# Performance work log

Measured on AMD Instinct MI355X. Metric: run time of the kernel, lower is better.

The kernel has to match this reference:

```python
import jax, jax.numpy as jnp
import numpy as np

L = 4          # decomposition_levels
PRUNE_Q = 0.4  # pruning_ratio


def haar_dwt2(img):
    a = img[:, 0::2, 0::2]; b = img[:, 0::2, 1::2]
    c = img[:, 1::2, 0::2]; d = img[:, 1::2, 1::2]
    cA = (a + b + c + d) * 0.5
    cH = (a - b + c - d) * 0.5
    cV = (a + b - c - d) * 0.5
    cD = (a - b - c + d) * 0.5
    return cA, cH, cV, cD


def haar_idwt2(cA, cH, cV, cD):
    # exact inverse of haar_dwt2: [B, h, w] -> [B, 2h, 2w]
    a = (cA + cH + cV + cD) * 0.5
    b = (cA - cH + cV - cD) * 0.5
    c = (cA + cH - cV - cD) * 0.5
    d = (cA - cH - cV + cD) * 0.5
    B, h, w = cA.shape
    top = jnp.stack([a, b], axis=-1).reshape(B, h, 2 * w)  # interleave cols
    bot = jnp.stack([c, d], axis=-1).reshape(B, h, 2 * w)
    return jnp.stack([top, bot], axis=2).reshape(B, 2 * h, 2 * w)  # interleave rows


def setup_inputs() -> dict:
    key = jax.random.key(0)
    k1, k2, k3 = jax.random.split(key, 3)
    B, in_dim, out_dim = 128, 4096, 4096
    x = jax.random.normal(k1, (B, in_dim), jnp.float32)
    base_weight = jax.random.normal(k2, (out_dim, in_dim), jnp.float32) * 0.02
    bias = jax.random.normal(k3, (out_dim,), jnp.float32) * 0.02
    scale_factors = jnp.ones((L, 4), jnp.float32)  # per-level, per-subband
    return {"x": x, "base_weight": base_weight, "bias": bias,
            "scale_factors": scale_factors}


def reference(x, base_weight, bias, scale_factors):
    B, in_dim = x.shape
    S = int(np.sqrt(in_dim))  # 64: each sample viewed as SxS image
    base_out = x @ base_weight.T  # [B, out_dim]

    # multi-level Haar analysis with per-level scaling + quantile pruning
    cA = x.reshape(B, S, S)
    levels = []
    for l in range(L):
        cA, cH, cV, cD = haar_dwt2(cA)
        co = jnp.stack([cA, cH, cV, cD], axis=1)  # [B, 4, h, w]
        co = co * scale_factors[l][None, :, None, None]
        ab = jnp.abs(co)
        thr = jnp.quantile(ab, PRUNE_Q, axis=-1, keepdims=True)
        co = co * (ab > thr).astype(co.dtype)
        levels.append(co)

    # synthesis from pruned coefficients
    rec = levels[-1][:, 0]  # coarsest pruned cA
    for l in range(L - 1, -1, -1):
        rec = haar_idwt2(rec, levels[l][:, 1], levels[l][:, 2], levels[l][:, 3])

    wavelet_out = rec.reshape(B, in_dim)  # out_dim == in_dim
    return base_out + wavelet_out + bias
```

## Files before the change

kernel.cpp:

```cpp
#include <hip/hip_runtime.h>
#include <hip/hip_bf16.h>

typedef __attribute__((ext_vector_type(8))) short bf16x8;
typedef __attribute__((ext_vector_type(4))) float f32x4;

__device__ __forceinline__ unsigned short f2bf(float f) {
  unsigned int u = __float_as_uint(f);
  u += 0x7FFFu + ((u >> 16) & 1u);
  return (unsigned short)(u >> 16);
}

__host__ __device__ constexpr int prOffset(int l) {
  return (l == 0) ? 0 : (l == 1) ? 3072 : (l == 2) ? 3840 : 4032;
}

template<int N>
__device__ __forceinline__ float row_thr(const float* __restrict__ row, float sc) {
  float v[N];
#pragma unroll
  for (int j = 0; j < N; ++j) v[j] = fabsf(row[j] * sc);
  constexpr float p = 0.4f * (float)(N - 1);
  constexpr int k = (int)p;
  constexpr float frac = p - (float)k;
  float vlo = 0.f, vhi = 0.f;
  for (int i = 0; i < N; ++i) {
    const float vi = fabsf(row[i] * sc);
    int clt = 0, ceq = 0;
#pragma unroll
    for (int j = 0; j < N; ++j) {
      clt += (v[j] < vi) ? 1 : 0;
      ceq += (v[j] == vi) ? 1 : 0;
    }
    if (clt <= k && k < clt + ceq) vlo = vi;
    if (clt <= k + 1 && (k + 1) < clt + ceq) vhi = vi;
  }
  return vlo * (1.0f - frac) + vhi * frac;
}

__global__ __launch_bounds__(256) void wavelet_kernel(
    const float* __restrict__ x,
    const float* __restrict__ bias,
    const float* __restrict__ scl,
    float* __restrict__ out) {
  __shared__ float cur[4096];
  __shared__ float tmp[4096];
  __shared__ float pr[4096];
  const int b = blockIdx.x;
  const int tid = threadIdx.x;
  const float* xi = x + (size_t)b * 4096;

  for (int i = tid; i < 4096; i += 256) cur[i] = xi[i];
  __syncthreads();

  int h = 64;
#pragma unroll
  for (int l = 0; l < 4; ++l) {
    const int half = h >> 1;
    const int hh = half * half;
    for (int e = tid; e < hh; e += 256) {
      const int i = e / half, j = e - i * half;
      const float a  = cur[(i * 2) * h + j * 2];
      const float bb = cur[(i * 2) * h + j * 2 + 1];
      const float c  = cur[(i * 2 + 1) * h + j * 2];
      const float d  = cur[(i * 2 + 1) * h + j * 2 + 1];
      tmp[e]          = (((a + bb) + c) + d) * 0.5f;
      tmp[hh + e]     = (((a - bb) + c) - d) * 0.5f;
      tmp[2 * hh + e] = (((a + bb) - c) - d) * 0.5f;
      tmp[3 * hh + e] = (((a - bb) - c) + d) * 0.5f;
    }
    __syncthreads();
    const int nrows = 4 * half;
    if (tid < nrows) {
      const int s = tid / half, i = tid - s * half;
      const float sc = scl[l * 4 + s];
      const float* row = &tmp[s * hh + i * half];
      float thr;
      if (half == 32)      thr = row_thr<32>(row, sc);
      else if (half == 16) thr = row_thr<16>(row, sc);
      else if (half == 8)  thr = row_thr<8>(row, sc);
      else                 thr = row_thr<4>(row, sc);
      float* dst = nullptr;
      if (s >= 1)          dst = &pr[prOffset(l) + (s - 1) * hh + i * half];
      else if (l == 3)     dst = &pr[4080 + i * 4];
      if (dst) {
        for (int j = 0; j < half; ++j) {
          const float co = row[j] * sc;
          dst[j] = (fabsf(co) > thr) ? co : 0.0f;
        }
      }
    }
    for (int e = tid; e < hh; e += 256) cur[e] = tmp[e];
    __syncthreads();
    h = half;
  }

#pragma unroll
  for (int l = 3; l >= 0; --l) {
    const int half = 64 >> (l + 1);
    const int hh = half * half;
    const int po = prOffset(l);
    const float* src = (l == 3) ? &pr[4080] : ((l & 1) ? tmp : cur);
    float* dst = (l & 1) ? cur : tmp;
    const int W2 = half * 2;
    for (int e = tid; e < hh; e += 256) {
      const int i = e / half, j = e - i * half;
      const float cA = src[e];
      const float cH = pr[po + 0 * hh + i * half + j];
      const float cV = pr[po + 1 * hh + i * half + j];
      const float cD = pr[po + 2 * hh + i * half + j];
      const float a2 = (((cA + cH) + cV) + cD) * 0.5f;
      const float b2 = (((cA - cH) + cV) - cD) * 0.5f;
      const float c2 = (((cA + cH) - cV) - cD) * 0.5f;
      const float d2 = (((cA - cH) - cV) + cD) * 0.5f;
      dst[(i * 2) * W2 + j * 2]         = a2;
      dst[(i * 2) * W2 + j * 2 + 1]     = b2;
      dst[(i * 2 + 1) * W2 + j * 2]     = c2;
      dst[(i * 2 + 1) * W2 + j * 2 + 1] = d2;
    }
    __syncthreads();
  }
  float* o = out + (size_t)b * 4096;
  for (int e = tid; e < 4096; e += 256) o[e] = tmp[e] + bias[e];
}

__global__ __launch_bounds__(256, 2) void gemm_kernel(
    const float* __restrict__ x,
    const float* __restrict__ w,
    float* __restrict__ out) {
  __shared__ __align__(16) unsigned short Asm[2][128][40];
  __shared__ __align__(16) unsigned short Bsm[2][64][40];
  const int tid = threadIdx.x;
  const int nt = blockIdx.x & 63;
  const int ks = blockIdx.x >> 6;
  const int n0 = nt * 64;
  const int k0 = ks * 512;
  const int q = tid & 7;
  const int r0 = tid >> 3;
  const int lane = tid & 63, wid = tid >> 6;
  const int wm = wid >> 1, wn = wid & 1;
  const int fr = lane & 15;
  const int k8 = (lane >> 4) * 8;

  f32x4 acc[4][2];
#pragma unroll
  for (int mi = 0; mi < 4; ++mi)
#pragma unroll
    for (int ni = 0; ni < 2; ++ni)
      acc[mi][ni] = f32x4{0.f, 0.f, 0.f, 0.f};

  float4 ra[4];
  float4 rb[2];
#pragma unroll
  for (int p = 0; p < 4; ++p)
    ra[p] = *(const float4*)&x[(size_t)(r0 + p * 32) * 4096 + k0 + q * 4];
#pragma unroll
  for (int p = 0; p < 2; ++p)
    rb[p] = *(const float4*)&w[(size_t)(n0 + r0 + p * 32) * 4096 + k0 + q * 4];
#pragma unroll
  for (int p = 0; p < 4; ++p) {
    ushort4 pk = {f2bf(ra[p].x), f2bf(ra[p].y), f2bf(ra[p].z), f2bf(ra[p].w)};
    *(ushort4*)&Asm[0][r0 + p * 32][q * 4] = pk;
  }
#pragma unroll
  for (int p = 0; p < 2; ++p) {
    ushort4 pk = {f2bf(rb[p].x), f2bf(rb[p].y), f2bf(rb[p].z), f2bf(rb[p].w)};
    *(ushort4*)&Bsm[0][r0 + p * 32][q * 4] = pk;
  }
  __syncthreads();

  for (int t = 0; t < 16; ++t) {
    const int cb = t & 1;
    if (t < 15) {
      const int kg = k0 + (t + 1) * 32;
#pragma unroll
      for (int p = 0; p < 4; ++p)
        ra[p] = *(const float4*)&x[(size_t)(r0 + p * 32) * 4096 + kg + q * 4];
#pragma unroll
      for (int p = 0; p < 2; ++p)
        rb[p] = *(const float4*)&w[(size_t)(n0 + r0 + p * 32) * 4096 + kg + q * 4];
    }
    bf16x8 af[4], bg[2];
#pragma unroll
    for (int mi = 0; mi < 4; ++mi)
      af[mi] = *(const bf16x8*)&Asm[cb][wm * 64 + mi * 16 + fr][k8];
#pragma unroll
    for (int ni = 0; ni < 2; ++ni)
      bg[ni] = *(const bf16x8*)&Bsm[cb][wn * 32 + ni * 16 + fr][k8];
#pragma unroll
    for (int mi = 0; mi < 4; ++mi)
#pragma unroll
      for (int ni = 0; ni < 2; ++ni)
        acc[mi][ni] = __builtin_amdgcn_mfma_f32_16x16x32_bf16(
            af[mi], bg[ni], acc[mi][ni], 0, 0, 0);
    if (t < 15) {
#pragma unroll
      for (int p = 0; p < 4; ++p) {
        ushort4 pk = {f2bf(ra[p].x), f2bf(ra[p].y), f2bf(ra[p].z), f2bf(ra[p].w)};
        *(ushort4*)&Asm[cb ^ 1][r0 + p * 32][q * 4] = pk;
      }
#pragma unroll
      for (int p = 0; p < 2; ++p) {
        ushort4 pk = {f2bf(rb[p].x), f2bf(rb[p].y), f2bf(rb[p].z), f2bf(rb[p].w)};
        *(ushort4*)&Bsm[cb ^ 1][r0 + p * 32][q * 4] = pk;
      }
    }
    __syncthreads();
  }

  const int rbase = wm * 64 + (lane >> 4) * 4;
  const int cbase = n0 + wn * 32 + fr;
#pragma unroll
  for (int mi = 0; mi < 4; ++mi)
#pragma unroll
    for (int ni = 0; ni < 2; ++ni)
#pragma unroll
      for (int j = 0; j < 4; ++j)
        atomicAdd(&out[(size_t)(rbase + mi * 16 + j) * 4096 + cbase + ni * 16],
                  acc[mi][ni][j]);
}

extern "C" void kernel_launch(void* const* d_in, const int* in_sizes, int n_in,
                              void* d_out, int out_size, void* d_ws, size_t ws_size,
                              hipStream_t stream) {
  const float* x    = (const float*)d_in[0];
  const float* w    = (const float*)d_in[1];
  const float* bias = (const float*)d_in[2];
  const float* scl  = (const float*)d_in[3];
  float* out = (float*)d_out;
  hipLaunchKernelGGL(wavelet_kernel, dim3(128), dim3(256), 0, stream,
                     x, bias, scl, out);
  hipLaunchKernelGGL(gemm_kernel, dim3(512), dim3(256), 0, stream,
                     x, w, out);
}
```

Before: 155.5 us.

## Parallelize quantile thresholds and add LDS-free GEMM on pre-converted bf16 activations

The per-row quantile threshold, previously one thread per row doing an O(N^2) rank count, is now spread across all 256 threads: each thread ranks a few elements and the row's low and high order statistics are written to shared memory. The wavelet kernel also writes a bf16 copy of x into the workspace, which a new GEMM kernel reads straight from global memory into MFMA fragments. That kernel converts weights with packed cvt instructions and uses no shared memory or barriers. This aims to cut the serial threshold latency and the LDS staging and conversion overhead in the GEMM, in exchange for a GEMM that now depends on the wavelet kernel and needs enough workspace.

```diff
diff --git a/kernel.cpp b/kernel.cpp
--- a/kernel.cpp
+++ b/kernel.cpp
@@ -10,89 +10,115 @@
   return (unsigned short)(u >> 16);
 }
 
+__device__ __forceinline__ bf16x8 pack8(float4 lo, float4 hi) {
+  union { unsigned int u[4]; bf16x8 v; } r;
+  asm("v_cvt_pk_bf16_f32 %0, %1, %2" : "=v"(r.u[0]) : "v"(lo.x), "v"(lo.y));
+  asm("v_cvt_pk_bf16_f32 %0, %1, %2" : "=v"(r.u[1]) : "v"(lo.z), "v"(lo.w));
+  asm("v_cvt_pk_bf16_f32 %0, %1, %2" : "=v"(r.u[2]) : "v"(hi.x), "v"(hi.y));
+  asm("v_cvt_pk_bf16_f32 %0, %1, %2" : "=v"(r.u[3]) : "v"(hi.z), "v"(hi.w));
+  return r.v;
+}
+
 __host__ __device__ constexpr int prOffset(int l) {
   return (l == 0) ? 0 : (l == 1) ? 3072 : (l == 2) ? 3840 : 4032;
 }
 
-template<int N>
-__device__ __forceinline__ float row_thr(const float* __restrict__ row, float sc) {
-  float v[N];
-#pragma unroll
-  for (int j = 0; j < N; ++j) v[j] = fabsf(row[j] * sc);
-  constexpr float p = 0.4f * (float)(N - 1);
-  constexpr int k = (int)p;
-  constexpr float frac = p - (float)k;
-  float vlo = 0.f, vhi = 0.f;
-  for (int i = 0; i < N; ++i) {
-    const float vi = fabsf(row[i] * sc);
-    int clt = 0, ceq = 0;
-#pragma unroll
-    for (int j = 0; j < N; ++j) {
-      clt += (v[j] < vi) ? 1 : 0;
-      ceq += (v[j] == vi) ? 1 : 0;
-    }
-    if (clt <= k && k < clt + ceq) vlo = vi;
-    if (clt <= k + 1 && (k + 1) < clt + ceq) vhi = vi;
-  }
-  return vlo * (1.0f - frac) + vhi * frac;
-}
-
-__global__ __launch_bounds__(256) void wavelet_kernel(
-    const float* __restrict__ x,
-    const float* __restrict__ bias,
-    const float* __restrict__ scl,
-    float* __restrict__ out) {
-  __shared__ float cur[4096];
-  __shared__ float tmp[4096];
-  __shared__ float pr[4096];
-  const int b = blockIdx.x;
-  const int tid = threadIdx.x;
-  const float* xi = x + (size_t)b * 4096;
-
-  for (int i = tid; i < 4096; i += 256) cur[i] = xi[i];
-  __syncthreads();
-
-  int h = 64;
-#pragma unroll
-  for (int l = 0; l < 4; ++l) {
-    const int half = h >> 1;
-    const int hh = half * half;
-    for (int e = tid; e < hh; e += 256) {
-      const int i = e / half, j = e - i * half;
-      const float a  = cur[(i * 2) * h + j * 2];
-      const float bb = cur[(i * 2) * h + j * 2 + 1];
-      const float c  = cur[(i * 2 + 1) * h + j * 2];
-      const float d  = cur[(i * 2 + 1) * h + j * 2 + 1];
-      tmp[e]          = (((a + bb) + c) + d) * 0.5f;
-      tmp[hh + e]     = (((a - bb) + c) - d) * 0.5f;
-      tmp[2 * hh + e] = (((a + bb) - c) - d) * 0.5f;
-      tmp[3 * hh + e] = (((a - bb) - c) + d) * 0.5f;
-    }
-    __syncthreads();
-    const int nrows = 4 * half;
-    if (tid < nrows) {
-      const int s = tid / half, i = tid - s * half;
-      const float sc = scl[l * 4 + s];
-      const float* row = &tmp[s * hh + i * half];
-      float thr;
-      if (half == 32)      thr = row_thr<32>(row, sc);
-      else if (half == 16) thr = row_thr<16>(row, sc);
-      else if (half == 8)  thr = row_thr<8>(row, sc);
-      else                 thr = row_thr<4>(row, sc);
-      float* dst = nullptr;
-      if (s >= 1)          dst = &pr[prOffset(l) + (s - 1) * hh + i * half];
-      else if (l == 3)     dst = &pr[4080 + i * 4];
-      if (dst) {
-        for (int j = 0; j < half; ++j) {
-          const float co = row[j] * sc;
-          dst[j] = (fabsf(co) > thr) ? co : 0.0f;
+template<int L>
+__device__ __forceinline__ void level_fwd(float* cur, float* tmp, float* ab,
+                                          float* pr, float* thrL, float* thrH,
+                                          const float* __restrict__ scl, int tid) {
+  constexpr int HALF = 32 >> L, LOG2 = 5 - L, HH = HALF * HALF, TOT = 4 * HH;
+  constexpr int H = HALF * 2;
+  constexpr float P = 0.4f * (float)(HALF - 1);
+  constexpr int K = (int)P;
+  constexpr float FRAC = P - (float)K;
+  const float s0 = scl[4 * L + 0], s1 = scl[4 * L + 1];
+  const float s2 = scl[4 * L + 2], s3 = scl[4 * L + 3];
+  for (int e = tid; e < HH; e += 256) {
+    const int i = e >> LOG2, j = e & (HALF - 1);
+    const float a = cur[(i * 2) * H + j * 2];
+    const float b = cur[(i * 2) * H + j * 2 + 1];
+    const float c = cur[(i * 2 + 1) * H + j * 2];
+    const float d = cur[(i * 2 + 1) * H + j * 2 + 1];
+    tmp[e]          = (((a + b) + c) + d) * 0.5f;
+    tmp[HH + e]     = (((a - b) + c) - d) * 0.5f;
+    tmp[2 * HH + e] = (((a + b) - c) - d) * 0.5f;
+    tmp[3 * HH + e] = (((a - b) - c) + d) * 0.5f;
+  }
+  __syncthreads();
+  for (int e = tid; e < TOT; e += 256) {
+    const int s = e >> (2 * LOG2);
+    const float sc = (s < 2) ? (s == 0 ? s0 : s1) : (s == 2 ? s2 : s3);
+    ab[e] = fabsf(tmp[e] * sc);
+  }
+  __syncthreads();
+  constexpr int CH = (TOT >= 256) ? TOT / 256 : 1;
+  {
+    const int base = tid * CH;
+    if (base < TOT) {
+      const int rowbase = base & ~(HALF - 1);
+      float v[CH]; int clt[CH], ceq[CH];
+#pragma unroll
+      for (int c = 0; c < CH; ++c) { v[c] = ab[base + c]; clt[c] = 0; ceq[c] = 0; }
+#pragma unroll
+      for (int rr = 0; rr < HALF; ++rr) {
+        const float a = ab[rowbase + rr];
+#pragma unroll
+        for (int c = 0; c < CH; ++c) {
+          clt[c] += (a < v[c]) ? 1 : 0;
+          ceq[c] += (a == v[c]) ? 1 : 0;
         }
       }
-    }
-    for (int e = tid; e < hh; e += 256) cur[e] = tmp[e];
-    __syncthreads();
-    h = half;
-  }
+      const int row = base >> LOG2;
+#pragma unroll
+      for (int c = 0; c < CH; ++c) {
+        if (clt[c] <= K && K < clt[c] + ceq[c]) thrL[row] = v[c];
+        if (clt[c] <= K + 1 && K + 1 < clt[c] + ceq[c]) thrH[row] = v[c];
+      }
+    }
+  }
+  __syncthreads();
+  for (int e = tid; e < TOT; e += 256) {
+    const int s = e >> (2 * LOG2);
+    const int row = e >> LOG2;
+    const float sc = (s < 2) ? (s == 0 ? s0 : s1) : (s == 2 ? s2 : s3);
+    const float thr = thrL[row] * (1.0f - FRAC) + thrH[row] * FRAC;
+    const float co = tmp[e] * sc;
+    const float val = (fabsf(co) > thr) ? co : 0.0f;
+    if (s >= 1) pr[prOffset(L) + e - HH] = val;
+    else {
+      if (L == 3) pr[4080 + e] = val;
+      cur[e] = tmp[e];
+    }
+  }
+  __syncthreads();
+}
+
+__global__ __launch_bounds__(256) void wavelet_kernel(
+    const float* __restrict__ x, const float* __restrict__ bias,
+    const float* __restrict__ scl, float* __restrict__ out,
+    unsigned short* __restrict__ xb, int writeXb) {
+  __shared__ float sh[16384];
+  float* cur = sh;
+  float* tmp = sh + 4096;
+  float* ab  = sh + 8192;
+  float* pr  = sh + 12288;
+  float* thrL = cur + 2048;
+  float* thrH = cur + 2176;
+  const int b = blockIdx.x, tid = threadIdx.x;
+  const float* xi = x + (size_t)b * 4096;
+
+  for (int i = tid; i < 4096; i += 256) {
+    const float v = xi[i];
+    cur[i] = v;
+    if (writeXb) xb[(size_t)b * 4096 + i] = f2bf(v);
+  }
+  __syncthreads();
+
+  level_fwd<0>(cur, tmp, ab, pr, thrL, thrH, scl, tid);
+  level_fwd<1>(cur, tmp, ab, pr, thrL, thrH, scl, tid);
+  level_fwd<2>(cur, tmp, ab, pr, thrL, thrH, scl, tid);
+  level_fwd<3>(cur, tmp, ab, pr, thrL, thrH, scl, tid);
 
 #pragma unroll
   for (int l = 3; l >= 0; --l) {
@@ -123,33 +149,80 @@
   for (int e = tid; e < 4096; e += 256) o[e] = tmp[e] + bias[e];
 }
 
+__global__ __launch_bounds__(256, 2) void gemm_ws(
+    const unsigned short* __restrict__ xb, const float* __restrict__ w,
+    float* __restrict__ out) {
+  const int tid = threadIdx.x, lane = tid & 63, wv = tid >> 6;
+  const int fr = lane & 15, k8 = (lane >> 4) * 8;
+  const int nt = blockIdx.x & 63, ks = blockIdx.x >> 6;
+  const int n0 = nt * 64, k0 = ks * 512;
+  const float* wr = w + (size_t)(n0 + wv * 16 + fr) * 4096 + k0 + k8;
+  const unsigned short* xr = xb + (size_t)fr * 4096 + k0 + k8;
+
+  f32x4 acc[8];
+#pragma unroll
+  for (int mi = 0; mi < 8; ++mi) acc[mi] = f32x4{0.f, 0.f, 0.f, 0.f};
+
+  float4 bfr[4][2];
+  bf16x8 afr[2][8];
+#pragma unroll
+  for (int p = 0; p < 4; ++p) {
+    bfr[p][0] = *(const float4*)(wr + p * 32);
+    bfr[p][1] = *(const float4*)(wr + p * 32 + 4);
+  }
+#pragma unroll
+  for (int p = 0; p < 2; ++p)
+#pragma unroll
+    for (int mi = 0; mi < 8; ++mi)
+      afr[p][mi] = *(const bf16x8*)(xr + mi * 16 * 4096 + p * 32);
+
+#pragma unroll
+  for (int t = 0; t < 16; ++t) {
+    const bf16x8 bb = pack8(bfr[t & 3][0], bfr[t & 3][1]);
+#pragma unroll
+    for (int mi = 0; mi < 8; ++mi)
+      acc[mi] = __builtin_amdgcn_mfma_f32_16x16x32_bf16(afr[t & 1][mi], bb,
+                                                        acc[mi], 0, 0, 0);
+    if (t < 12) {
+      bfr[t & 3][0] = *(const float4*)(wr + (t + 4) * 32);
+      bfr[t & 3][1] = *(const float4*)(wr + (t + 4) * 32 + 4);
+    }
+    if (t < 14) {
+#pragma unroll
+      for (int mi = 0; mi < 8; ++mi)
+        afr[t & 1][mi] = *(const bf16x8*)(xr + mi * 16 * 4096 + (t + 2) * 32);
+    }
+  }
+
+  const int rq = (lane >> 4) * 4;
+  const int col = n0 + wv * 16 + fr;
+#pragma unroll
+  for (int mi = 0; mi < 8; ++mi)
+#pragma unroll
+    for (int j = 0; j < 4; ++j)
+      atomicAdd(&out[(size_t)(mi * 16 + rq + j) * 4096 + col], acc[mi][j]);
+}
+
 __global__ __launch_bounds__(256, 2) void gemm_kernel(
-    const float* __restrict__ x,
-    const float* __restrict__ w,
+    const float* __restrict__ x, const float* __restrict__ w,
     float* __restrict__ out) {
   __shared__ __align__(16) unsigned short Asm[2][128][40];
   __shared__ __align__(16) unsigned short Bsm[2][64][40];
   const int tid = threadIdx.x;
-  const int nt = blockIdx.x & 63;
-  const int ks = blockIdx.x >> 6;
-  const int n0 = nt * 64;
-  const int k0 = ks * 512;
-  const int q = tid & 7;
-  const int r0 = tid >> 3;
+  const int nt = blockIdx.x & 63, ks = blockIdx.x >> 6;
+  const int n0 = nt * 64, k0 = ks * 512;
+  const int q = tid & 7, r0 = tid >> 3;
   const int lane = tid & 63, wid = tid >> 6;
   const int wm = wid >> 1, wn = wid & 1;
-  const int fr = lane & 15;
-  const int k8 = (lane >> 4) * 8;
+  const int fr = lane & 15, k8 = (lane >> 4) * 8;
 
   f32x4 acc[4][2];
 #pragma unroll
   for (int mi = 0; mi < 4; ++mi)
 #pragma unroll
-    for (int ni = 0; ni < 2; ++ni)
-      acc[mi][ni] = f32x4{0.f, 0.f, 0.f, 0.f};
-
-  float4 ra[4];
-  float4 rb[2];
+    for (int ni = 0; ni < 2; ++ni) acc[mi][ni] = f32x4{0.f, 0.f, 0.f, 0.f};
+
+  float4 ra[4]; float4 rb[2];
 #pragma unroll
   for (int p = 0; p < 4; ++p)
     ra[p] = *(const float4*)&x[(size_t)(r0 + p * 32) * 4096 + k0 + q * 4];
@@ -190,8 +263,8 @@
     for (int mi = 0; mi < 4; ++mi)
 #pragma unroll
       for (int ni = 0; ni < 2; ++ni)
-        acc[mi][ni] = __builtin_amdgcn_mfma_f32_16x16x32_bf16(
-            af[mi], bg[ni], acc[mi][ni], 0, 0, 0);
+        acc[mi][ni] = __builtin_amdgcn_mfma_f32_16x16x32_bf16(af[mi], bg[ni],
+                                                              acc[mi][ni], 0, 0, 0);
     if (t < 15) {
 #pragma unroll
       for (int p = 0; p < 4; ++p) {
@@ -227,8 +300,12 @@
   const float* bias = (const float*)d_in[2];
   const float* scl  = (const float*)d_in[3];
   float* out = (float*)d_out;
+  const bool useWs = ws_size >= (size_t)128 * 4096 * 2;
+  unsigned short* xbp = (unsigned short*)d_ws;
   hipLaunchKernelGGL(wavelet_kernel, dim3(128), dim3(256), 0, stream,
-                     x, bias, scl, out);
-  hipLaunchKernelGGL(gemm_kernel, dim3(512), dim3(256), 0, stream,
-                     x, w, out);
-}
+                     x, bias, scl, out, xbp, useWs ? 1 : 0);
+  if (useWs)
+    hipLaunchKernelGGL(gemm_ws, dim3(512), dim3(256), 0, stream, xbp, w, out);
+  else
+    hipLaunchKernelGGL(gemm_kernel, dim3(512), dim3(256), 0, stream, x, w, out);
+}
```

New measurement: 153.5 us. Within noise of the previous version (-1.3%).
